# Performance work log

Hardware: AMD Instinct MI355X
Metric: run time of the kernel (lower is better)

Reference implementation:

```python
import jax, jax.numpy as jnp
import numpy as np

B = 65536      # batch (groups of time steps)
T = 5          # time_step
OBS = 128      # unit-data feature dim
ACT = 32       # action feature dim
H = 64         # n_hidden
EPS = 1e-12    # tf.contrib layer_norm epsilon
FORGET_BIAS = 1.0


def _ln_last(x, g, b):
    # layer norm over last axis (2D inputs in the TF graph)
    m = jnp.mean(x, axis=-1, keepdims=True)
    v = jnp.mean(jnp.square(x - m), axis=-1, keepdims=True)
    return (x - m) * jax.lax.rsqrt(v + EPS) * g + b


def _ln_all_but_batch(x, g, b):
    # tf.contrib.layers.layer_norm on 3D input: normalize over axes (1,2), params on last axis
    m = jnp.mean(x, axis=(1, 2), keepdims=True)
    v = jnp.mean(jnp.square(x - m), axis=(1, 2), keepdims=True)
    return (x - m) * jax.lax.rsqrt(v + EPS) * g + b


def _rev_seq(x, au):
    # tf.reverse_sequence along time axis 1 with per-batch lengths au
    t = jnp.arange(T)[None, :]
    idx = jnp.where(t < au[:, None], au[:, None] - 1 - t, t)  # [B, T]
    return jnp.take_along_axis(x, idx[:, :, None], axis=1)


def _lstm(x_btc, au, kernel, bias):
    # BasicLSTMCell (gates i, j, f, o) with sequence_length semantics:
    # past the length, outputs are zero and state is copied through.
    x_tbc = jnp.transpose(x_btc, (1, 0, 2))  # [T, B, C]
    Bn = x_tbc.shape[1]
    c0 = jnp.zeros((Bn, H), x_btc.dtype)
    h0 = jnp.zeros((Bn, H), x_btc.dtype)

    def step(carry, inp):
        c, h = carry
        x_t, t = inp
        valid = (t < au)[:, None]
        gates = jnp.concatenate([x_t, h], axis=-1) @ kernel + bias
        i, j, f, o = jnp.split(gates, 4, axis=-1)
        new_c = jax.nn.sigmoid(f + FORGET_BIAS) * c + jax.nn.sigmoid(i) * jnp.tanh(j)
        new_h = jax.nn.sigmoid(o) * jnp.tanh(new_c)
        c = jnp.where(valid, new_c, c)
        h_carry = jnp.where(valid, new_h, h)
        out = jnp.where(valid, new_h, 0.0)
        return (c, h_carry), out

    (_, _), ys = jax.lax.scan(step, (c0, h0), (x_tbc, jnp.arange(T)))
    return jnp.transpose(ys, (1, 0, 2))  # [B, T, H]


def setup_inputs() -> dict:
    key = jax.random.key(0)
    ks = jax.random.split(key, 12)
    s = 0.05
    return {
        "ud": jax.random.normal(ks[0], (B * T, OBS), jnp.float32),
        "action": jax.random.normal(ks[1], (B * T, ACT), jnp.float32),
        "mask": jax.random.uniform(ks[2], (B, T), jnp.float32),
        "ln0_g": jnp.ones((OBS,), jnp.float32), "ln0_b": jnp.zeros((OBS,), jnp.float32),
        "W1": jax.random.normal(ks[3], (OBS, H), jnp.float32) * s, "b1": jnp.zeros((H,), jnp.float32),
        "ln1_g": jnp.ones((H,), jnp.float32), "ln1_b": jnp.zeros((H,), jnp.float32),
        "W2": jax.random.normal(ks[4], (H + ACT, H), jnp.float32) * s, "b2": jnp.zeros((H,), jnp.float32),
        "ln2_g": jnp.ones((H,), jnp.float32), "ln2_b": jnp.zeros((H,), jnp.float32),
        "fw_k": jax.random.normal(ks[5], (2 * H, 4 * H), jnp.float32) * s,
        "fw_b": jnp.zeros((4 * H,), jnp.float32),
        "bw_k": jax.random.normal(ks[6], (2 * H, 4 * H), jnp.float32) * s,
        "bw_b": jnp.zeros((4 * H,), jnp.float32),
        "ln3_g": jnp.ones((2 * H,), jnp.float32), "ln3_b": jnp.zeros((2 * H,), jnp.float32),
        "conv_w": jax.random.uniform(ks[7], (2 * H,), jnp.float32, -0.003, 0.003),
        "conv_b": jnp.zeros((), jnp.float32),
        "au": jax.random.randint(ks[8], (B,), 1, T + 1, jnp.int32),
    }


def reference(ud, action, mask, ln0_g, ln0_b, W1, b1, ln1_g, ln1_b, W2, b2,
              ln2_g, ln2_b, fw_k, fw_b, bw_k, bw_b, ln3_g, ln3_b,
              conv_w, conv_b, au):
    x = _ln_last(ud, ln0_g, ln0_b)
    x = x @ W1 + b1
    x = jax.nn.relu(_ln_last(x, ln1_g, ln1_b))
    x = jnp.concatenate([x, action], axis=-1)
    x = x @ W2 + b2
    x = jax.nn.relu(_ln_last(x, ln2_g, ln2_b))
    x = x.reshape(B, T, H)
    fw = _lstm(x, au, fw_k, fw_b)
    bw = _rev_seq(_lstm(_rev_seq(x, au), au, bw_k, bw_b), au)
    x = jnp.concatenate([fw, bw], axis=2)                     # [B, T, 2H]
    x = jax.nn.relu(_ln_all_but_batch(x, ln3_g, ln3_b))
    # conv1d with kernel_size=stride=2H on [B, T*2H, 1] == per-step dot product
    q = jnp.einsum('btc,c->bt', x, conv_w) + conv_b           # [B, T]
    Q_mask = q * mask
    Q = jnp.sum(Q_mask, axis=1, keepdims=True)                # [B, 1]
    return Q


if __name__ == "__main__":
    out = reference(**setup_inputs())
    print(out.shape)
```

## Files before the change

kernel.cpp:

```cpp
#include <hip/hip_runtime.h>
#include <hip/hip_bf16.h>

#define NB    65536
#define NT    5
#define NOBS  128
#define NACT  32
#define NH    64

typedef __attribute__((ext_vector_type(8))) short bf16x8;
typedef __attribute__((ext_vector_type(4))) float f32x4;

__device__ __forceinline__ float sigf(float x) { return 1.0f / (1.0f + __expf(-x)); }
__device__ __forceinline__ float tanh_fast(float x) { return 1.0f - 2.0f / (__expf(2.0f * x) + 1.0f); }

__device__ __forceinline__ unsigned short f2b(float x) {
  __hip_bfloat16 h = __float2bfloat16(x);
  return *(unsigned short*)&h;
}
__device__ __forceinline__ float b2f(unsigned short u) {
  __hip_bfloat16 h = *(__hip_bfloat16*)&u;
  return __bfloat162float(h);
}
__device__ __forceinline__ void split_bf16(float x, unsigned short& h, unsigned short& l) {
  h = f2b(x);
  l = f2b(x - b2f(h));
}

__global__ __launch_bounds__(256) void k0_prep(
    const float* __restrict__ fk, const float* __restrict__ bk,
    const float* __restrict__ W1, const float* __restrict__ W2,
    const float* __restrict__ ln0g, const float* __restrict__ ln0b,
    const float* __restrict__ b1,
    unsigned int* __restrict__ fkT, unsigned int* __restrict__ bkT,
    unsigned short* __restrict__ w1h, unsigned short* __restrict__ w1l,
    unsigned short* __restrict__ w2h, unsigned short* __restrict__ w2l,
    float* __restrict__ u1, float* __restrict__ vb1) {
  const int bx = blockIdx.x;
  if (bx < 64) {
    const int g  = threadIdx.x;
    const int k0 = bx * 2;
    unsigned int flo = f2b(fk[(k0 + 0) * 256 + g]);
    unsigned int fhi = f2b(fk[(k0 + 1) * 256 + g]);
    unsigned int blo = f2b(bk[(k0 + 0) * 256 + g]);
    unsigned int bhi = f2b(bk[(k0 + 1) * 256 + g]);
    fkT[g * 64 + bx] = flo | (fhi << 16);
    bkT[g * 64 + bx] = blo | (bhi << 16);
    return;
  }
  const int id = (bx - 64) * 256 + threadIdx.x;
  if (id < 1024) {
    const int f = id >> 6, l = id & 63;
    const int kb = f >> 2, nt = f & 3;
    const int q = l >> 4, l16 = l & 15;
    const int n = nt * 16 + l16;
    bf16x8 vh, vl;
#pragma unroll
    for (int j = 0; j < 8; ++j) {
      const int k = kb * 32 + q * 8 + j;
      float wg = ln0g[k] * W1[k * 64 + n];
      unsigned short h, lo;
      split_bf16(wg, h, lo);
      vh[j] = (short)h; vl[j] = (short)lo;
    }
    *(bf16x8*)&w1h[(f * 64 + l) * 8] = vh;
    *(bf16x8*)&w1l[(f * 64 + l) * 8] = vl;
  } else if (id < 1792) {
    const int f = (id - 1024) >> 6, l = id & 63;
    const int kb = f >> 2, nt = f & 3;
    const int q = l >> 4, l16 = l & 15;
    const int n = nt * 16 + l16;
    bf16x8 vh, vl;
#pragma unroll
    for (int j = 0; j < 8; ++j) {
      const int k = kb * 32 + q * 8 + j;
      float wv = W2[k * 64 + n];
      unsigned short h, lo;
      split_bf16(wv, h, lo);
      vh[j] = (short)h; vl[j] = (short)lo;
    }
    *(bf16x8*)&w2h[(f * 64 + l) * 8] = vh;
    *(bf16x8*)&w2l[(f * 64 + l) * 8] = vl;
  } else if (id < 1856) {
    const int n = id - 1792;
    float u = 0.0f, vb = 0.0f;
    for (int k = 0; k < 128; ++k) {
      float wv = W1[k * 64 + n];
      u  += ln0g[k] * wv;
      vb += ln0b[k] * wv;
    }
    u1[n]  = u;
    vb1[n] = vb + b1[n];
  }
}

__global__ __launch_bounds__(256, 2) void k1_mlp(
    const float* __restrict__ ud, const float* __restrict__ action,
    const unsigned short* __restrict__ w1h, const unsigned short* __restrict__ w1l,
    const unsigned short* __restrict__ w2h, const unsigned short* __restrict__ w2l,
    const float* __restrict__ u1, const float* __restrict__ vb1,
    const float* __restrict__ gb2, const float* __restrict__ ln1g,
    const float* __restrict__ ln1b, const float* __restrict__ ln2g,
    const float* __restrict__ ln2b,
    unsigned short* __restrict__ hin) {
  const int wave = threadIdx.x >> 6;
  const int lane = threadIdx.x & 63;
  const int quad = lane >> 4;
  const int l16  = lane & 15;
  const int base = (blockIdx.x * 4 + wave) * 16;

  __shared__ __align__(16) unsigned short lds[4][4][2048];
  unsigned short* xh  = &lds[wave][0][0];
  unsigned short* xl  = &lds[wave][1][0];
  unsigned short* x2h = &lds[wave][2][0];
  unsigned short* x2l = &lds[wave][3][0];

  float u1v[4], vbv[4], g1v[4], c1v[4], b2v[4], g2v[4], c2v[4];
#pragma unroll
  for (int nt = 0; nt < 4; ++nt) {
    const int col = nt * 16 + l16;
    u1v[nt] = u1[col];  vbv[nt] = vb1[col];
    g1v[nt] = ln1g[col]; c1v[nt] = ln1b[col];
    b2v[nt] = gb2[col];
    g2v[nt] = ln2g[col]; c2v[nt] = ln2b[col];
  }

  {
    const int arow = lane >> 2, ag = lane & 3;
    const float* ap = &action[(size_t)(base + arow) * NACT + ag * 8];
    float4 a0 = *(const float4*)ap;
    float4 a1 = *(const float4*)(ap + 4);
    float av[8] = {a0.x, a0.y, a0.z, a0.w, a1.x, a1.y, a1.z, a1.w};
    bf16x8 vh, vl;
#pragma unroll
    for (int j = 0; j < 8; ++j) {
      unsigned short h, lo;
      split_bf16(av[j], h, lo);
      vh[j] = (short)h; vl[j] = (short)lo;
    }
    const int idx = arow * 128 + (((8 + ag) ^ (arow & 15)) << 3);
    *(bf16x8*)&x2h[idx] = vh;
    *(bf16x8*)&x2l[idx] = vl;
  }

#pragma unroll
  for (int r = 0; r < 16; ++r) {
    float2 xx = *(const float2*)&ud[(size_t)(base + r) * NOBS + 2 * lane];
    unsigned short h0, l0, h1, l1;
    split_bf16(xx.x, h0, l0);
    split_bf16(xx.y, h1, l1);
    const int di = r * 64 + (((lane >> 2) ^ (r & 15)) << 2) + (lane & 3);
    ((unsigned int*)xh)[di] = (unsigned int)h0 | ((unsigned int)h1 << 16);
    ((unsigned int*)xl)[di] = (unsigned int)l0 | ((unsigned int)l1 << 16);
  }

  bf16x8 W1hf[16], W1lf[16];
#pragma unroll
  for (int f = 0; f < 16; ++f) {
    W1hf[f] = *(const bf16x8*)&w1h[(f * 64 + lane) * 8];
    W1lf[f] = *(const bf16x8*)&w1l[(f * 64 + lane) * 8];
  }

  bf16x8 ones;
#pragma unroll
  for (int j = 0; j < 8; ++j) ones[j] = (short)0x3F80;

  f32x4 acc[4], s_acc, q_acc;
#pragma unroll
  for (int nt = 0; nt < 4; ++nt) acc[nt] = 0.0f;
  s_acc = 0.0f; q_acc = 0.0f;

#pragma unroll
  for (int kb = 0; kb < 4; ++kb) {
    const int ai = l16 * 128 + (((kb * 4 + quad) ^ l16) << 3);
    bf16x8 Ah = *(const bf16x8*)&xh[ai];
    bf16x8 Al = *(const bf16x8*)&xl[ai];
    bf16x8 Asq;
#pragma unroll
    for (int j = 0; j < 8; ++j) {
      unsigned int uu = ((unsigned int)(unsigned short)Ah[j]) << 16;
      float v = __uint_as_float(uu);
      v *= v;
      Asq[j] = (short)(unsigned short)(__float_as_uint(v) >> 16);
    }
    s_acc = __builtin_amdgcn_mfma_f32_16x16x32_bf16(Ah, ones, s_acc, 0, 0, 0);
    s_acc = __builtin_amdgcn_mfma_f32_16x16x32_bf16(Al, ones, s_acc, 0, 0, 0);
    q_acc = __builtin_amdgcn_mfma_f32_16x16x32_bf16(Asq, ones, q_acc, 0, 0, 0);
#pragma unroll
    for (int nt = 0; nt < 4; ++nt) {
      const int f = kb * 4 + nt;
      acc[nt] = __builtin_amdgcn_mfma_f32_16x16x32_bf16(Ah, W1hf[f], acc[nt], 0, 0, 0);
      acc[nt] = __builtin_amdgcn_mfma_f32_16x16x32_bf16(Ah, W1lf[f], acc[nt], 0, 0, 0);
      acc[nt] = __builtin_amdgcn_mfma_f32_16x16x32_bf16(Al, W1hf[f], acc[nt], 0, 0, 0);
    }
  }

  float inv0[4], ivm[4];
#pragma unroll
  for (int r = 0; r < 4; ++r) {
    float m   = s_acc[r] * (1.0f / 128.0f);
    float var = q_acc[r] * (1.0f / 128.0f) - m * m;
    float inv = rsqrtf(var + 1e-12f);
    inv0[r] = inv;
    ivm[r]  = inv * m;
  }
  float y[4][4];
#pragma unroll
  for (int nt = 0; nt < 4; ++nt)
#pragma unroll
    for (int r = 0; r < 4; ++r)
      y[nt][r] = fmaf(inv0[r], acc[nt][r], fmaf(-ivm[r], u1v[nt], vbv[nt]));

  float m1[4], i1[4];
#pragma unroll
  for (int r = 0; r < 4; ++r) {
    float s1 = y[0][r] + y[1][r] + y[2][r] + y[3][r];
    float q1 = y[0][r] * y[0][r] + y[1][r] * y[1][r] +
               y[2][r] * y[2][r] + y[3][r] * y[3][r];
#pragma unroll
    for (int off = 1; off <= 8; off <<= 1) {
      s1 += __shfl_xor(s1, off, 64);
      q1 += __shfl_xor(q1, off, 64);
    }
    float mm = s1 * (1.0f / 64.0f);
    m1[r] = mm;
    i1[r] = rsqrtf(q1 * (1.0f / 64.0f) - mm * mm + 1e-12f);
  }

#pragma unroll
  for (int nt = 0; nt < 4; ++nt)
#pragma unroll
    for (int r = 0; r < 4; ++r) {
      float x1 = fmaxf(0.0f, fmaf((y[nt][r] - m1[r]) * i1[r], g1v[nt], c1v[nt]));
      unsigned short h, lo;
      split_bf16(x1, h, lo);
      const int row = quad * 4 + r;
      const int idx = row * 128 + (((nt * 2 + (l16 >> 3)) ^ (row & 15)) << 3) + (l16 & 7);
      x2h[idx] = h;
      x2l[idx] = lo;
    }

  f32x4 acc2[4];
#pragma unroll
  for (int nt = 0; nt < 4; ++nt) acc2[nt] = 0.0f;

#pragma unroll
  for (int kb = 0; kb < 3; ++kb) {
    bf16x8 w2hf[4], w2lf[4];
#pragma unroll
    for (int nt = 0; nt < 4; ++nt) {
      const int f = kb * 4 + nt;
      w2hf[nt] = *(const bf16x8*)&w2h[(f * 64 + lane) * 8];
      w2lf[nt] = *(const bf16x8*)&w2l[(f * 64 + lane) * 8];
    }
    const int ai = l16 * 128 + (((kb * 4 + quad) ^ l16) << 3);
    bf16x8 Ah = *(const bf16x8*)&x2h[ai];
    bf16x8 Al = *(const bf16x8*)&x2l[ai];
#pragma unroll
    for (int nt = 0; nt < 4; ++nt) {
      acc2[nt] = __builtin_amdgcn_mfma_f32_16x16x32_bf16(Ah, w2hf[nt], acc2[nt], 0, 0, 0);
      acc2[nt] = __builtin_amdgcn_mfma_f32_16x16x32_bf16(Ah, w2lf[nt], acc2[nt], 0, 0, 0);
      acc2[nt] = __builtin_amdgcn_mfma_f32_16x16x32_bf16(Al, w2hf[nt], acc2[nt], 0, 0, 0);
    }
  }

  float y2[4][4];
#pragma unroll
  for (int nt = 0; nt < 4; ++nt)
#pragma unroll
    for (int r = 0; r < 4; ++r)
      y2[nt][r] = acc2[nt][r] + b2v[nt];

  float m2[4], i2[4];
#pragma unroll
  for (int r = 0; r < 4; ++r) {
    float s2 = y2[0][r] + y2[1][r] + y2[2][r] + y2[3][r];
    float q2 = y2[0][r] * y2[0][r] + y2[1][r] * y2[1][r] +
               y2[2][r] * y2[2][r] + y2[3][r] * y2[3][r];
#pragma unroll
    for (int off = 1; off <= 8; off <<= 1) {
      s2 += __shfl_xor(s2, off, 64);
      q2 += __shfl_xor(q2, off, 64);
    }
    float mm = s2 * (1.0f / 64.0f);
    m2[r] = mm;
    i2[r] = rsqrtf(q2 * (1.0f / 64.0f) - mm * mm + 1e-12f);
  }

#pragma unroll
  for (int nt = 0; nt < 4; ++nt)
#pragma unroll
    for (int r = 0; r < 4; ++r) {
      float o = fmaxf(0.0f, fmaf((y2[nt][r] - m2[r]) * i2[r], g2v[nt], c2v[nt]));
      const int row = quad * 4 + r;
      hin[(size_t)(base + row) * NH + nt * 16 + l16] = f2b(o);
    }
}

__global__ __launch_bounds__(256) void k2_lstm(
    const unsigned short* __restrict__ hin,
    const unsigned short* __restrict__ fkT, const float* __restrict__ fwb,
    const unsigned short* __restrict__ bkT, const float* __restrict__ bwb,
    const int* __restrict__ au,
    unsigned short* __restrict__ fwout, unsigned short* __restrict__ bwout) {
  const int tid  = threadIdx.x;
  const int w    = tid >> 6;
  const int lane = tid & 63;
  const int quad = lane >> 4;
  const int l16  = lane & 15;
  const int dir  = blockIdx.y;
  const int batch0 = blockIdx.x * 64;

  __shared__ __align__(16) unsigned short xA[64 * 128];
  __shared__ int au_s[64];

  const unsigned short* kT   = dir ? bkT : fkT;
  const float*          bias = dir ? bwb : fwb;
  unsigned short*       out  = dir ? bwout : fwout;

  if (tid < 64) au_s[tid] = au[batch0 + tid];
  for (int i = tid; i < 64 * 128 / 2; i += 256) ((unsigned int*)xA)[i] = 0u;

  bf16x8 Bf[4][4];
#pragma unroll
  for (int g = 0; g < 4; ++g) {
    const int n = g * 64 + w * 16 + l16;
#pragma unroll
    for (int kb = 0; kb < 4; ++kb)
      Bf[g][kb] = *(const bf16x8*)&kT[n * 128 + kb * 32 + quad * 8];
  }
  const int u = w * 16 + l16;
  float bg0 = bias[u], bg1 = bias[64 + u], bg2 = bias[128 + u], bg3 = bias[192 + u];

  __syncthreads();

  int aur[16];
#pragma unroll
  for (int mt = 0; mt < 4; ++mt)
#pragma unroll
    for (int r = 0; r < 4; ++r)
      aur[mt * 4 + r] = au_s[mt * 16 + quad * 4 + r];

  float c_s[16], h_s[16];
#pragma unroll
  for (int i = 0; i < 16; ++i) { c_s[i] = 0.0f; h_s[i] = 0.0f; }

  for (int t = 0; t < NT; ++t) {
#pragma unroll
    for (int rep = 0; rep < 2; ++rep) {
      int r = (tid >> 3) + rep * 32;
      int c8 = tid & 7;
      int alen = au_s[r];
      int st = (dir == 0) ? t : ((t < alen) ? (alen - 1 - t) : t);
      float4 v = *(const float4*)&hin[((batch0 + r) * NT + st) * NH + c8 * 8];
      *(float4*)&xA[r * 128 + ((c8 ^ (r & 15)) << 3)] = v;
    }
    __syncthreads();

    f32x4 acc[4][4];
#pragma unroll
    for (int mt = 0; mt < 4; ++mt)
#pragma unroll
      for (int g = 0; g < 4; ++g) acc[mt][g] = 0.0f;

#pragma unroll
    for (int mt = 0; mt < 4; ++mt) {
      const int m = mt * 16 + l16;
      bf16x8 Af[4];
#pragma unroll
      for (int kb = 0; kb < 4; ++kb)
        Af[kb] = *(const bf16x8*)&xA[m * 128 + (((kb * 4 + quad) ^ l16) << 3)];
#pragma unroll
      for (int g = 0; g < 4; ++g)
#pragma unroll
        for (int kb = 0; kb < 4; ++kb)
          acc[mt][g] = __builtin_amdgcn_mfma_f32_16x16x32_bf16(Af[kb], Bf[g][kb],
                                                               acc[mt][g], 0, 0, 0);
    }
    __syncthreads();

#pragma unroll
    for (int mt = 0; mt < 4; ++mt) {
#pragma unroll
      for (int r = 0; r < 4; ++r) {
        const int idx = mt * 4 + r;
        const int bl = mt * 16 + quad * 4 + r;
        const int b = batch0 + bl;
        float gi = acc[mt][0][r] + bg0;
        float gj = acc[mt][1][r] + bg1;
        float gf = acc[mt][2][r] + bg2;
        float go = acc[mt][3][r] + bg3;
        float nc = sigf(gf + 1.0f) * c_s[idx] + sigf(gi) * tanh_fast(gj);
        float nh = sigf(go) * tanh_fast(nc);
        bool valid = t < aur[idx];
        c_s[idx] = valid ? nc : c_s[idx];
        h_s[idx] = valid ? nh : h_s[idx];
        float outv = valid ? nh : 0.0f;
        int pos = (dir == 0) ? t : ((t < aur[idx]) ? (aur[idx] - 1 - t) : t);
        out[(b * NT + pos) * NH + u] = f2b(outv);
        const int e = 64 + u;
        xA[bl * 128 + (((e >> 3) ^ (bl & 15)) << 3) + (e & 7)] = f2b(h_s[idx]);
      }
    }
    __syncthreads();
  }
}

__global__ __launch_bounds__(256) void k3_final(
    const unsigned short* __restrict__ fwout, const unsigned short* __restrict__ bwout,
    const float* __restrict__ ln3g, const float* __restrict__ ln3b,
    const float* __restrict__ conv_w, const float* __restrict__ conv_b,
    const float* __restrict__ mask, float* __restrict__ out) {
  const int wave = threadIdx.x >> 6;
  const int lane = threadIdx.x & 63;
  const int b = blockIdx.x * 4 + wave;

  float f[NT], w[NT];
#pragma unroll
  for (int t = 0; t < NT; ++t) {
    f[t] = b2f(fwout[(b * NT + t) * NH + lane]);
    w[t] = b2f(bwout[(b * NT + t) * NH + lane]);
  }
  float s = 0.0f, q = 0.0f;
#pragma unroll
  for (int t = 0; t < NT; ++t) {
    s += f[t] + w[t];
    q += f[t] * f[t] + w[t] * w[t];
  }
#pragma unroll
  for (int off = 32; off; off >>= 1) {
    s += __shfl_xor(s, off, 64);
    q += __shfl_xor(q, off, 64);
  }
  float m = s * (1.0f / 640.0f);
  float var = q * (1.0f / 640.0f) - m * m;
  float inv = rsqrtf(var + 1e-12f);

  const float gl = ln3g[lane], gh = ln3g[64 + lane];
  const float bl = ln3b[lane], bh = ln3b[64 + lane];
  const float cwl = conv_w[lane], cwh = conv_w[64 + lane];
  const float cb = conv_b[0];

  float Q = 0.0f;
#pragma unroll
  for (int t = 0; t < NT; ++t) {
    float xf = fmaxf((f[t] - m) * inv * gl + bl, 0.0f);
    float xb = fmaxf((w[t] - m) * inv * gh + bh, 0.0f);
    float p = xf * cwl + xb * cwh;
#pragma unroll
    for (int off = 32; off; off >>= 1) p += __shfl_xor(p, off, 64);
    float qv = p + cb;
    Q += qv * mask[b * NT + t];
  }
  if (lane == 0) out[b] = Q;
}

extern "C" void kernel_launch(void* const* d_in, const int* in_sizes, int n_in,
                              void* d_out, int out_size, void* d_ws, size_t ws_size,
                              hipStream_t stream) {
  const float* ud     = (const float*)d_in[0];
  const float* action = (const float*)d_in[1];
  const float* mask   = (const float*)d_in[2];
  const float* ln0g   = (const float*)d_in[3];
  const float* ln0b   = (const float*)d_in[4];
  const float* W1     = (const float*)d_in[5];
  const float* b1     = (const float*)d_in[6];
  const float* ln1g   = (const float*)d_in[7];
  const float* ln1b   = (const float*)d_in[8];
  const float* W2     = (const float*)d_in[9];
  const float* b2     = (const float*)d_in[10];
  const float* ln2g   = (const float*)d_in[11];
  const float* ln2b   = (const float*)d_in[12];
  const float* fwk    = (const float*)d_in[13];
  const float* fwb    = (const float*)d_in[14];
  const float* bwk    = (const float*)d_in[15];
  const float* bwb    = (const float*)d_in[16];
  const float* ln3g   = (const float*)d_in[17];
  const float* ln3b   = (const float*)d_in[18];
  const float* conv_w = (const float*)d_in[19];
  const float* conv_b = (const float*)d_in[20];
  const int*   au     = (const int*)d_in[21];

  const size_t n_hin = (size_t)NB * NT * NH;
  unsigned short* wsu   = (unsigned short*)d_ws;
  unsigned short* hin   = wsu;
  unsigned short* fwout = hin + n_hin;
  unsigned short* bwout = fwout + n_hin;
  unsigned short* fkT   = bwout + n_hin;
  unsigned short* bkT   = fkT + 32768;
  unsigned short* w1h   = bkT + 32768;
  unsigned short* w1l   = w1h + 8192;
  unsigned short* w2h   = w1l + 8192;
  unsigned short* w2l   = w2h + 6144;
  float*          u1    = (float*)(w2l + 6144);
  float*          vb1   = u1 + 64;

  float* outf = (float*)d_out;

  k0_prep<<<72, 256, 0, stream>>>(fwk, bwk, W1, W2, ln0g, ln0b, b1,
                                  (unsigned int*)fkT, (unsigned int*)bkT,
                                  w1h, w1l, w2h, w2l, u1, vb1);
  k1_mlp<<<(NB * NT) / 64, 256, 0, stream>>>(ud, action, w1h, w1l, w2h, w2l,
                                             u1, vb1, b2, ln1g, ln1b, ln2g, ln2b,
                                             hin);
  k2_lstm<<<dim3(NB / 64, 2), 256, 0, stream>>>(hin, fkT, fwb, bkT, bwb, au,
                                                fwout, bwout);
  k3_final<<<NB / 4, 256, 0, stream>>>(fwout, bwout, ln3g, ln3b, conv_w, conv_b,
                                       mask, outf);
}
```

Baseline: 525.3 us.

## Fuse bidirectional LSTM with final layernorm/conv reduction, keep outputs in LDS

Merges the LSTM and final reduction kernels. Each block now handles 32 batch rows and runs both directions in turn, keeping per-step outputs in shared memory instead of writing fw/bw outputs to global memory and reading them back. Input x fragments are loaded straight from global into registers, with a prefetch of the next step, and only h lives in a swizzled LDS tile. The conv bias term is folded as cb times the mask sum. In exchange, each block runs the two directions serially and uses about 45 KB of LDS, which may reduce occupancy.

Measured after the change: 520.4 us. No clear change (-0.9%).

```diff
diff --git a/kernel.cpp b/kernel.cpp
--- a/kernel.cpp
+++ b/kernel.cpp
@@ -296,162 +296,174 @@
     }
 }
 
-__global__ __launch_bounds__(256) void k2_lstm(
+__global__ __launch_bounds__(256, 2) void k23_lstm_final(
     const unsigned short* __restrict__ hin,
     const unsigned short* __restrict__ fkT, const float* __restrict__ fwb,
     const unsigned short* __restrict__ bkT, const float* __restrict__ bwb,
     const int* __restrict__ au,
-    unsigned short* __restrict__ fwout, unsigned short* __restrict__ bwout) {
+    const float* __restrict__ ln3g, const float* __restrict__ ln3b,
+    const float* __restrict__ conv_w, const float* __restrict__ conv_b,
+    const float* __restrict__ mask, float* __restrict__ out) {
   const int tid  = threadIdx.x;
   const int w    = tid >> 6;
   const int lane = tid & 63;
   const int quad = lane >> 4;
   const int l16  = lane & 15;
-  const int dir  = blockIdx.y;
-  const int batch0 = blockIdx.x * 64;
-
-  __shared__ __align__(16) unsigned short xA[64 * 128];
-  __shared__ int au_s[64];
-
-  const unsigned short* kT   = dir ? bkT : fkT;
-  const float*          bias = dir ? bwb : fwb;
-  unsigned short*       out  = dir ? bwout : fwout;
-
-  if (tid < 64) au_s[tid] = au[batch0 + tid];
-  for (int i = tid; i < 64 * 128 / 2; i += 256) ((unsigned int*)xA)[i] = 0u;
-
-  bf16x8 Bf[4][4];
-#pragma unroll
-  for (int g = 0; g < 4; ++g) {
-    const int n = g * 64 + w * 16 + l16;
-#pragma unroll
-    for (int kb = 0; kb < 4; ++kb)
-      Bf[g][kb] = *(const bf16x8*)&kT[n * 128 + kb * 32 + quad * 8];
-  }
+  const int batch0 = blockIdx.x * 32;
+
+  __shared__ __align__(16) unsigned short obuf[10 * 32 * 64];
+  __shared__ __align__(16) unsigned short hA[32 * 64];
+
   const int u = w * 16 + l16;
-  float bg0 = bias[u], bg1 = bias[64 + u], bg2 = bias[128 + u], bg3 = bias[192 + u];
-
-  __syncthreads();
-
-  int aur[16];
-#pragma unroll
-  for (int mt = 0; mt < 4; ++mt)
+
+  const int aum0 = au[batch0 + l16];
+  const int aum1 = au[batch0 + 16 + l16];
+  int aur[8];
+#pragma unroll
+  for (int mt = 0; mt < 2; ++mt)
 #pragma unroll
     for (int r = 0; r < 4; ++r)
-      aur[mt * 4 + r] = au_s[mt * 16 + quad * 4 + r];
-
-  float c_s[16], h_s[16];
-#pragma unroll
-  for (int i = 0; i < 16; ++i) { c_s[i] = 0.0f; h_s[i] = 0.0f; }
-
-  for (int t = 0; t < NT; ++t) {
-#pragma unroll
-    for (int rep = 0; rep < 2; ++rep) {
-      int r = (tid >> 3) + rep * 32;
-      int c8 = tid & 7;
-      int alen = au_s[r];
-      int st = (dir == 0) ? t : ((t < alen) ? (alen - 1 - t) : t);
-      float4 v = *(const float4*)&hin[((batch0 + r) * NT + st) * NH + c8 * 8];
-      *(float4*)&xA[r * 128 + ((c8 ^ (r & 15)) << 3)] = v;
-    }
+      aur[mt * 4 + r] = au[batch0 + mt * 16 + quad * 4 + r];
+
+  for (int dir = 0; dir < 2; ++dir) {
+    const unsigned short* kT   = dir ? bkT : fkT;
+    const float*          bias = dir ? bwb : fwb;
+
+    bf16x8 Bf[4][4];
+#pragma unroll
+    for (int g = 0; g < 4; ++g) {
+      const int n = g * 64 + u;
+#pragma unroll
+      for (int kb = 0; kb < 4; ++kb)
+        Bf[g][kb] = *(const bf16x8*)&kT[n * 128 + kb * 32 + quad * 8];
+    }
+    const float bg0 = bias[u], bg1 = bias[64 + u];
+    const float bg2 = bias[128 + u], bg3 = bias[192 + u];
+
     __syncthreads();
-
-    f32x4 acc[4][4];
-#pragma unroll
-    for (int mt = 0; mt < 4; ++mt)
-#pragma unroll
-      for (int g = 0; g < 4; ++g) acc[mt][g] = 0.0f;
-
-#pragma unroll
-    for (int mt = 0; mt < 4; ++mt) {
+    *(float4*)&hA[tid * 8] = make_float4(0.f, 0.f, 0.f, 0.f);
+    float c_s[8], h_s[8];
+#pragma unroll
+    for (int i = 0; i < 8; ++i) { c_s[i] = 0.0f; h_s[i] = 0.0f; }
+    __syncthreads();
+
+    bf16x8 Ax0[2], Ax1[2];
+#pragma unroll
+    for (int mt = 0; mt < 2; ++mt) {
       const int m = mt * 16 + l16;
-      bf16x8 Af[4];
-#pragma unroll
-      for (int kb = 0; kb < 4; ++kb)
-        Af[kb] = *(const bf16x8*)&xA[m * 128 + (((kb * 4 + quad) ^ l16) << 3)];
-#pragma unroll
-      for (int g = 0; g < 4; ++g)
-#pragma unroll
-        for (int kb = 0; kb < 4; ++kb)
-          acc[mt][g] = __builtin_amdgcn_mfma_f32_16x16x32_bf16(Af[kb], Bf[g][kb],
-                                                               acc[mt][g], 0, 0, 0);
-    }
-    __syncthreads();
-
-#pragma unroll
-    for (int mt = 0; mt < 4; ++mt) {
-#pragma unroll
-      for (int r = 0; r < 4; ++r) {
-        const int idx = mt * 4 + r;
-        const int bl = mt * 16 + quad * 4 + r;
-        const int b = batch0 + bl;
-        float gi = acc[mt][0][r] + bg0;
-        float gj = acc[mt][1][r] + bg1;
-        float gf = acc[mt][2][r] + bg2;
-        float go = acc[mt][3][r] + bg3;
-        float nc = sigf(gf + 1.0f) * c_s[idx] + sigf(gi) * tanh_fast(gj);
-        float nh = sigf(go) * tanh_fast(nc);
-        bool valid = t < aur[idx];
-        c_s[idx] = valid ? nc : c_s[idx];
-        h_s[idx] = valid ? nh : h_s[idx];
-        float outv = valid ? nh : 0.0f;
-        int pos = (dir == 0) ? t : ((t < aur[idx]) ? (aur[idx] - 1 - t) : t);
-        out[(b * NT + pos) * NH + u] = f2b(outv);
-        const int e = 64 + u;
-        xA[bl * 128 + (((e >> 3) ^ (bl & 15)) << 3) + (e & 7)] = f2b(h_s[idx]);
+      const int a = mt ? aum1 : aum0;
+      const int st = dir ? (a - 1) : 0;
+      const size_t rb = ((size_t)(batch0 + m) * NT + st) * NH;
+      Ax0[mt] = *(const bf16x8*)&hin[rb + quad * 8];
+      Ax1[mt] = *(const bf16x8*)&hin[rb + 32 + quad * 8];
+    }
+
+    for (int t = 0; t < NT; ++t) {
+      f32x4 acc[2][4];
+#pragma unroll
+      for (int mt = 0; mt < 2; ++mt)
+#pragma unroll
+        for (int g = 0; g < 4; ++g) acc[mt][g] = 0.0f;
+
+#pragma unroll
+      for (int mt = 0; mt < 2; ++mt) {
+        const int m = mt * 16 + l16;
+        bf16x8 Ah0 = *(const bf16x8*)&hA[m * 64 + ((quad ^ (m & 7)) << 3)];
+        bf16x8 Ah1 = *(const bf16x8*)&hA[m * 64 + (((4 + quad) ^ (m & 7)) << 3)];
+#pragma unroll
+        for (int g = 0; g < 4; ++g) {
+          acc[mt][g] = __builtin_amdgcn_mfma_f32_16x16x32_bf16(Ax0[mt], Bf[g][0], acc[mt][g], 0, 0, 0);
+          acc[mt][g] = __builtin_amdgcn_mfma_f32_16x16x32_bf16(Ax1[mt], Bf[g][1], acc[mt][g], 0, 0, 0);
+          acc[mt][g] = __builtin_amdgcn_mfma_f32_16x16x32_bf16(Ah0, Bf[g][2], acc[mt][g], 0, 0, 0);
+          acc[mt][g] = __builtin_amdgcn_mfma_f32_16x16x32_bf16(Ah1, Bf[g][3], acc[mt][g], 0, 0, 0);
+        }
       }
-    }
-    __syncthreads();
-  }
-}
-
-__global__ __launch_bounds__(256) void k3_final(
-    const unsigned short* __restrict__ fwout, const unsigned short* __restrict__ bwout,
-    const float* __restrict__ ln3g, const float* __restrict__ ln3b,
-    const float* __restrict__ conv_w, const float* __restrict__ conv_b,
-    const float* __restrict__ mask, float* __restrict__ out) {
-  const int wave = threadIdx.x >> 6;
-  const int lane = threadIdx.x & 63;
-  const int b = blockIdx.x * 4 + wave;
-
-  float f[NT], w[NT];
-#pragma unroll
-  for (int t = 0; t < NT; ++t) {
-    f[t] = b2f(fwout[(b * NT + t) * NH + lane]);
-    w[t] = b2f(bwout[(b * NT + t) * NH + lane]);
-  }
-  float s = 0.0f, q = 0.0f;
-#pragma unroll
-  for (int t = 0; t < NT; ++t) {
-    s += f[t] + w[t];
-    q += f[t] * f[t] + w[t] * w[t];
-  }
-#pragma unroll
-  for (int off = 32; off; off >>= 1) {
-    s += __shfl_xor(s, off, 64);
-    q += __shfl_xor(q, off, 64);
-  }
-  float m = s * (1.0f / 640.0f);
-  float var = q * (1.0f / 640.0f) - m * m;
-  float inv = rsqrtf(var + 1e-12f);
-
-  const float gl = ln3g[lane], gh = ln3g[64 + lane];
-  const float bl = ln3b[lane], bh = ln3b[64 + lane];
-  const float cwl = conv_w[lane], cwh = conv_w[64 + lane];
-  const float cb = conv_b[0];
-
-  float Q = 0.0f;
-#pragma unroll
-  for (int t = 0; t < NT; ++t) {
-    float xf = fmaxf((f[t] - m) * inv * gl + bl, 0.0f);
-    float xb = fmaxf((w[t] - m) * inv * gh + bh, 0.0f);
-    float p = xf * cwl + xb * cwh;
-#pragma unroll
-    for (int off = 32; off; off >>= 1) p += __shfl_xor(p, off, 64);
-    float qv = p + cb;
-    Q += qv * mask[b * NT + t];
-  }
-  if (lane == 0) out[b] = Q;
+
+      if (t < NT - 1) {
+        const int t2 = t + 1;
+#pragma unroll
+        for (int mt = 0; mt < 2; ++mt) {
+          const int m = mt * 16 + l16;
+          const int a = mt ? aum1 : aum0;
+          const int st = dir ? ((t2 < a) ? (a - 1 - t2) : t2) : t2;
+          const size_t rb = ((size_t)(batch0 + m) * NT + st) * NH;
+          Ax0[mt] = *(const bf16x8*)&hin[rb + quad * 8];
+          Ax1[mt] = *(const bf16x8*)&hin[rb + 32 + quad * 8];
+        }
+      }
+
+      __syncthreads();
+
+#pragma unroll
+      for (int mt = 0; mt < 2; ++mt) {
+#pragma unroll
+        for (int r = 0; r < 4; ++r) {
+          const int idx = mt * 4 + r;
+          const int bl = mt * 16 + quad * 4 + r;
+          float gi = acc[mt][0][r] + bg0;
+          float gj = acc[mt][1][r] + bg1;
+          float gf = acc[mt][2][r] + bg2;
+          float go = acc[mt][3][r] + bg3;
+          float nc = sigf(gf + 1.0f) * c_s[idx] + sigf(gi) * tanh_fast(gj);
+          float nh = sigf(go) * tanh_fast(nc);
+          bool valid = t < aur[idx];
+          c_s[idx] = valid ? nc : c_s[idx];
+          h_s[idx] = valid ? nh : h_s[idx];
+          float outv = valid ? nh : 0.0f;
+          int pos = dir ? ((t < aur[idx]) ? (aur[idx] - 1 - t) : t) : t;
+          obuf[(dir * 5 + pos) * 2048 + bl * 64 + u] = f2b(outv);
+          hA[bl * 64 + (((u >> 3) ^ (bl & 7)) << 3) + (u & 7)] = f2b(h_s[idx]);
+        }
+      }
+      __syncthreads();
+    }
+  }
+
+  const float gl  = ln3g[lane],      gh  = ln3g[64 + lane];
+  const float bl3 = ln3b[lane],      bh3 = ln3b[64 + lane];
+  const float cwl = conv_w[lane],    cwh = conv_w[64 + lane];
+  const float cb  = conv_b[0];
+
+  for (int bb = w * 8; bb < w * 8 + 8; ++bb) {
+    const int b = batch0 + bb;
+    float v0[NT], v1[NT];
+#pragma unroll
+    for (int p = 0; p < NT; ++p) {
+      v0[p] = b2f(obuf[p * 2048 + bb * 64 + lane]);
+      v1[p] = b2f(obuf[(5 + p) * 2048 + bb * 64 + lane]);
+    }
+    float s = 0.0f, q = 0.0f;
+#pragma unroll
+    for (int p = 0; p < NT; ++p) {
+      s += v0[p] + v1[p];
+      q += v0[p] * v0[p] + v1[p] * v1[p];
+    }
+#pragma unroll
+    for (int off = 32; off; off >>= 1) {
+      s += __shfl_xor(s, off, 64);
+      q += __shfl_xor(q, off, 64);
+    }
+    float m = s * (1.0f / 640.0f);
+    float var = q * (1.0f / 640.0f) - m * m;
+    float inv = rsqrtf(var + 1e-12f);
+
+    float mk[NT], masksum = 0.0f;
+#pragma unroll
+    for (int p = 0; p < NT; ++p) {
+      mk[p] = mask[b * NT + p];
+      masksum += mk[p];
+    }
+    float local = 0.0f;
+#pragma unroll
+    for (int p = 0; p < NT; ++p) {
+      float xf = fmaxf(0.0f, (v0[p] - m) * inv * gl + bl3);
+      float xb = fmaxf(0.0f, (v1[p] - m) * inv * gh + bh3);
+      local += mk[p] * (xf * cwl + xb * cwh);
+    }
+#pragma unroll
+    for (int off = 32; off; off >>= 1) local += __shfl_xor(local, off, 64);
+    if (lane == 0) out[b] = local + cb * masksum;
+  }
 }
 
 extern "C" void kernel_launch(void* const* d_in, const int* in_sizes, int n_in,
@@ -483,9 +495,7 @@
   const size_t n_hin = (size_t)NB * NT * NH;
   unsigned short* wsu   = (unsigned short*)d_ws;
   unsigned short* hin   = wsu;
-  unsigned short* fwout = hin + n_hin;
-  unsigned short* bwout = fwout + n_hin;
-  unsigned short* fkT   = bwout + n_hin;
+  unsigned short* fkT   = hin + n_hin;
   unsigned short* bkT   = fkT + 32768;
   unsigned short* w1h   = bkT + 32768;
   unsigned short* w1l   = w1h + 8192;
@@ -502,8 +512,7 @@
   k1_mlp<<<(NB * NT) / 64, 256, 0, stream>>>(ud, action, w1h, w1l, w2h, w2l,
                                              u1, vb1, b2, ln1g, ln1b, ln2g, ln2b,
                                              hin);
-  k2_lstm<<<dim3(NB / 64, 2), 256, 0, stream>>>(hin, fkT, fwb, bkT, bwb, au,
-                                                fwout, bwout);
-  k3_final<<<NB / 4, 256, 0, stream>>>(fwout, bwout, ln3g, ln3b, conv_w, conv_b,
-                                       mask, outf);
-}
+  k23_lstm_final<<<NB / 32, 256, 0, stream>>>(hin, fkT, fwb, bkT, bwb, au,
+                                              ln3g, ln3b, conv_w, conv_b,
+                                              mask, outf);
+}
```
